# Kernel tuning notes

Hardware: AMD Instinct MI355X
Metric: run time of the kernel (lower is better)

Reference implementation:

```python
import jax, jax.numpy as jnp
import numpy as np

S = 3        # num_scale
C = 256      # codebook / feature dim
K = 512      # codebook size


def _bilinear_down(x, f):
    # torch F.interpolate(scale_factor=1/f, mode='bilinear', align_corners=False)
    # for even integer f: src = (i+0.5)*f - 0.5 = f*i + (f//2 - 1) + 0.5 -> avg of 2 neighbors.
    o = f // 2 - 1
    x = (x[:, :, o::f, :] + x[:, :, o + 1::f, :]) * 0.5
    x = (x[:, :, :, o::f] + x[:, :, :, o + 1::f]) * 0.5
    return x


def _encode(img, w, b):
    # stride-4 patchify conv: (b,3,H,W) -> (b,C,H/4,W/4), NCHW
    y = jax.lax.conv_general_dilated(img, w, (4, 4), 'VALID',
                                     dimension_numbers=('NCHW', 'OIHW', 'NCHW'))
    return y + b[None, :, None, None]


def _match(e, cb):
    # e [..., c], cb [K, c]. logits = -||e - cb||^2; zsoft = softmax(logits).
    # Only max-prob and argmax are consumed downstream, so compute them stably.
    d = (jnp.sum(e * e, -1, keepdims=True)
         - 2.0 * jnp.einsum('...c,kc->...k', e, cb)
         + jnp.sum(cb * cb, -1))
    logits = -d
    zidx = jnp.argmax(logits, -1)
    maxprob = jnp.exp(jnp.max(logits, -1) - jax.scipy.special.logsumexp(logits, -1))
    return maxprob, zidx


def _resample(e, j, i):
    # e is NHWC at scale j; bring it to scale i (avg_pool if j<i, nearest upsample if j>i)
    if j == i:
        return e
    if j < i:
        f = 2 ** (i - j)
        b, h, w, c = e.shape
        return e.reshape(b, h // f, f, w // f, f, c).mean(axis=(2, 4))
    f = 2 ** (j - i)
    return jnp.repeat(jnp.repeat(e, f, axis=1), f, axis=2)


def setup_inputs() -> dict:
    key = jax.random.key(0)
    k1, k2, k3 = jax.random.split(key, 3)
    image = jax.random.normal(k1, (8, 3, 256, 256), jnp.float32)
    conv_w = jax.random.normal(k2, (C, 3, 4, 4), jnp.float32) * 0.05
    conv_b = jnp.zeros((C,), jnp.float32)
    codebooks = jax.random.normal(k3, (1 + S, K, C), jnp.float32) * 0.05
    return {"image": image, "conv_w": conv_w, "conv_b": conv_b, "codebooks": codebooks}


def reference(image, conv_w, conv_b, codebooks):
    # multi-scale inputs (bilinear downsample), shared encoder per scale
    imgs = [image] + [_bilinear_down(image, 2 ** k) for k in range(1, S)]
    encodes = [_encode(im, conv_w, conv_b) for im in imgs]          # NCHW, sizes 64/32/16
    enc_nhwc = [jnp.transpose(e, (0, 2, 3, 1)) for e in encodes]

    cb0 = codebooks[0]
    # ms_fuse, scale i1 = 0 (only scale 0 is returned when decode=None, retr=True):
    stack = jnp.stack([_resample(enc_nhwc[j], j, 0) for j in range(S)])  # [s,b,h,w,c]
    prob1, idx1 = _match(stack, cb0)                                      # [s,b,h,w]
    sel = jnp.argmax(prob1, 0)                                            # [b,h,w] best scale
    zidx1 = jnp.take_along_axis(idx1, sel[None], 0)[0]                    # [b,h,w]
    enc1 = jnp.take_along_axis(stack, sel[None, ..., None], 0)[0]         # [b,h,w,c]
    quant1 = cb0[zidx1]

    # per-scale quantizer for scale 0
    _, zidx2 = _match(enc_nhwc[0], codebooks[1])
    quant2 = codebooks[1][zidx2]

    zidx0 = jnp.stack([zidx1, zidx2], -1)            # [b,h,w,2]
    e_fused = (enc1 + enc_nhwc[0]) * 0.5
    q_fused = (quant1 + quant2) * 0.5
    # alpha = 0 -> residual == quant; naive STE
    ste0 = e_fused + jax.lax.stop_gradient(q_fused - e_fused)

    return (encodes[0],
            jnp.transpose(zidx0, (0, 3, 1, 2)),
            jnp.transpose(ste0, (0, 3, 1, 2)))
```

## Files before the change

### kernel.cpp

```cpp
#include <hip/hip_runtime.h>
#include <math.h>


#define FEAT_OFF   0
#define PART_OFF   11010048
#define PROB_OFF   13434880
#define IDX1_OFF   13477888
#define IDX2_OFF   13520896
#define CNF_OFF    13553664
#define CND_OFF    13554688
#define CBS_OFF    13556736
#define IMG1_OFF   13818880
#define IMG2_OFF   14212096
#define RLIST_OFF  14310400
#define DLIST_OFF  14386176
#define CNT_OFF    14418944

#define PLANE_STRIDE 11010048

#define EPS_V 1e-3f
#define EPS_P_REL 2e-3f

typedef __attribute__((ext_vector_type(8))) short short8;
typedef __attribute__((ext_vector_type(4))) float f32x4;

__device__ inline unsigned short f2bf(float x) {
    unsigned u = __float_as_uint(x);
    return (unsigned short)((u + 0x7FFFu + ((u >> 16) & 1u)) >> 16);
}
__device__ inline float bf2f(unsigned short h) {
    return __uint_as_float(((unsigned)h) << 16);
}
__device__ inline int rswz(int row) { return (row & 3) ^ ((row >> 2) & 3); }

__device__ inline void glds16(const unsigned short* g, unsigned short* l) {
    __builtin_amdgcn_global_load_lds(
        (const __attribute__((address_space(1))) void*)g,
        (__attribute__((address_space(3))) void*)l, 16, 0, 0);
}

__global__ void zero_cnt(int* cnt) { if (threadIdx.x < 2) cnt[threadIdx.x] = 0; }

__global__ void ds_kernel(const float* __restrict__ img, float* __restrict__ out,
                          int Hout, int Wout, int o, int f) {
    int i = blockIdx.x * blockDim.x + threadIdx.x;
    if (i >= 8 * 3 * Hout * Wout) return;
    int x = i % Wout;
    int t = i / Wout;
    int y = t % Hout;
    int bc = t / Hout;
    const float* base = img + ((size_t)bc * 256 + (size_t)(y * f + o)) * 256;
    int cx = x * f + o;
    float v00 = base[cx],     v10 = base[256 + cx];
    float v01 = base[cx + 1], v11 = base[256 + cx + 1];
    out[i] = ((v00 + v10) * 0.5f + (v01 + v11) * 0.5f) * 0.5f;
}

__global__ void cnorm_kernel(const float* __restrict__ cb, double* __restrict__ cnd,
                             float* __restrict__ cnf) {
    int row = blockIdx.x;
    const float* p = cb + (size_t)row * 256;
    int lane = threadIdx.x;
    double s = 0.0;
    for (int c = lane; c < 256; c += 64) {
        double v = (double)p[c];
        s = fma(v, v, s);
    }
    #pragma unroll
    for (int off = 32; off; off >>= 1) s += __shfl_down(s, off);
    if (lane == 0) { cnd[row] = s; cnf[row] = (float)s; }
}

__global__ void split_cb(const float* __restrict__ codebooks, unsigned short* __restrict__ cbs) {
    int i = blockIdx.x * 256 + threadIdx.x;
    if (i >= 262144) return;
    int book = i >> 17, rem = i & 131071;
    int code = rem >> 8, ch = rem & 255;
    float c = codebooks[(size_t)book * 131072 + rem];
    unsigned short h0 = f2bf(c);
    unsigned short h1 = f2bf(c - bf2f(h0));
    int codeblk = code >> 7, row = code & 127;
    int kc = ch >> 5, q = (ch >> 3) & 3, j = ch & 7;
    int qs = q ^ rswz(row);
    size_t off = ((((size_t)(book * 2) * 4 + codeblk) * 8 + kc) * 128 + row) * 32 + qs * 8 + j;
    cbs[off] = h0;
    cbs[off + 4 * 32768] = h1;
}

__launch_bounds__(256)
__global__ void encode_all(const float* __restrict__ image,
                           const float* __restrict__ img1,
                           const float* __restrict__ img2,
                           const float* __restrict__ w,
                           const float* __restrict__ bias,
                           float* __restrict__ feat,
                           unsigned short* __restrict__ featbf) {
    __shared__ float patch[12 * 256];
    __shared__ __align__(16) unsigned short pk[2][2][256];
    int bid = blockIdx.x;
    const float* img; int Hout, rowbase, local;
    if (bid < 512)      { img = image; Hout = 64; rowbase = 0;     local = bid; }
    else if (bid < 768) { img = img1;  Hout = 32; rowbase = 32768; local = bid - 512; }
    else                { img = img2;  Hout = 16; rowbase = 40960; local = bid - 768; }
    int Wout = Hout;
    int tid = threadIdx.x;
    int b = local / Hout, y = local % Hout;
    int Himg = Hout * 4, Wimg = Wout * 4;

    const float* ibase = img + (size_t)b * 3 * Himg * Wimg;
    int nload = 12 * Wimg;
    for (int i = tid; i < nload; i += 256) {
        int col = i % Wimg, r = i / Wimg;
        int ci = r >> 2, kh = r & 3;
        patch[r * Wimg + col] = ibase[((size_t)ci * Himg + 4 * y + kh) * Wimg + col];
    }
    float wr[48];
    #pragma unroll
    for (int j = 0; j < 48; j++) wr[j] = w[tid * 48 + j];
    float bv = bias[tid];
    __syncthreads();

    int wp = tid >> 5, wkc = (tid >> 2) & 7, wg = tid & 3;
    int rb = rowbase + (b * Hout + y) * Wout;
    for (int x = 0; x < Wout; x++) {
        float acc = 0.f;
        #pragma unroll
        for (int ci = 0; ci < 3; ci++)
            #pragma unroll
            for (int kh = 0; kh < 4; kh++) {
                const float* pr = &patch[(ci * 4 + kh) * Wimg + 4 * x];
                #pragma unroll
                for (int kw = 0; kw < 4; kw++)
                    acc = fmaf(pr[kw], wr[ci * 16 + kh * 4 + kw], acc);
            }
        float val = acc + bv;
        int r = rb + x;
        feat[(size_t)r * 256 + tid] = val;
        unsigned short hi = f2bf(val);
        unsigned short lo = f2bf(val - bf2f(hi));
        int bufx = x & 1;
        pk[bufx][0][tid] = hi;
        pk[bufx][1][tid] = lo;
        __syncthreads();
        if (tid < 64) {
            int rowblk = r >> 7, rrow = r & 127;
            int ch0 = wkc * 32 + ((wg ^ rswz(rrow)) << 3);
            uint4 v = *(const uint4*)&pk[bufx][wp][ch0];
            size_t off = ((((size_t)rowblk * 8 + wkc) * 128 + rrow) * 32 + wg * 8)
                         + (size_t)wp * PLANE_STRIDE;
            *(uint4*)&featbf[off] = v;
        }
    }
}

__launch_bounds__(256, 2)
__global__ void match_bulk(const unsigned short* __restrict__ featbf,
                           const unsigned short* __restrict__ cbs,
                           const float* __restrict__ cnf,
                           float* __restrict__ partials) {
    __shared__ unsigned short A0s[2][4096], A1s[2][4096], B0s[2][4096], B1s[2][4096];
    int bid0 = blockIdx.x;
    int bid = (bid0 & 7) * 296 + (bid0 >> 3);
    int codeblk = bid & 3, rowtile = bid >> 2;
    int book = (rowtile >= 336) ? 1 : 0;
    int rowblk = book ? rowtile - 336 : rowtile;
    int vr0 = rowtile * 128;
    int tid = threadIdx.x;
    int wid = tid >> 6, l = tid & 63;
    int waveY = wid & 1, waveX = wid >> 1;
    int lm = l & 15, lq = l >> 4;
    int slot = lq ^ rswz(lm);
    int wlds = wid * 512;

    int kbase = codeblk * 128 + waveX * 64 + lq * 4;
    float4 cnv4[4];
    #pragma unroll
    for (int ct = 0; ct < 4; ct++)
        cnv4[ct] = *(const float4*)&cnf[book * 512 + kbase + ct * 16];

    f32x4 acc[4][4];
    #pragma unroll
    for (int ct = 0; ct < 4; ct++)
        #pragma unroll
        for (int rt = 0; rt < 4; rt++) acc[ct][rt] = (f32x4)0.0f;

    const unsigned short* gA0 = featbf + (size_t)rowblk * 32768 + tid * 8;
    const unsigned short* gA1 = gA0 + PLANE_STRIDE;
    const unsigned short* gB0 = cbs + ((size_t)(book * 8) + codeblk) * 32768 + tid * 8;
    const unsigned short* gB1 = gB0 + 4 * 32768;

    auto STAGE = [&](int buf, int kc) {
        const unsigned short* ga0 = gA0 + kc * 4096;
        const unsigned short* ga1 = gA1 + kc * 4096;
        const unsigned short* gb0 = gB0 + kc * 4096;
        const unsigned short* gb1 = gB1 + kc * 4096;
        #pragma unroll
        for (int i = 0; i < 2; i++) {
            glds16(ga0 + i * 2048, &A0s[buf][i * 2048 + wlds]);
            glds16(ga1 + i * 2048, &A1s[buf][i * 2048 + wlds]);
            glds16(gb0 + i * 2048, &B0s[buf][i * 2048 + wlds]);
            glds16(gb1 + i * 2048, &B1s[buf][i * 2048 + wlds]);
        }
    };

    short8 a0[4], a1[4], b0[4], b1[4];
    auto LOADFRAG = [&](int cur) {
        #pragma unroll
        for (int t = 0; t < 4; t++) {
            int ra = (waveY * 64 + t * 16 + lm) * 32 + slot * 8;
            int rbx = (waveX * 64 + t * 16 + lm) * 32 + slot * 8;
            a0[t] = *(const short8*)&A0s[cur][ra];
            a1[t] = *(const short8*)&A1s[cur][ra];
            b0[t] = *(const short8*)&B0s[cur][rbx];
            b1[t] = *(const short8*)&B1s[cur][rbx];
        }
    };
    auto DOMFMA = [&]() {
        __builtin_amdgcn_s_setprio(1);
        #pragma unroll
        for (int ct = 0; ct < 4; ct++)
            #pragma unroll
            for (int rt = 0; rt < 4; rt++) {
                acc[ct][rt] = __builtin_amdgcn_mfma_f32_16x16x32_bf16(b0[ct], a0[rt], acc[ct][rt], 0, 0, 0);
                acc[ct][rt] = __builtin_amdgcn_mfma_f32_16x16x32_bf16(b1[ct], a0[rt], acc[ct][rt], 0, 0, 0);
                acc[ct][rt] = __builtin_amdgcn_mfma_f32_16x16x32_bf16(b0[ct], a1[rt], acc[ct][rt], 0, 0, 0);
            }
        __builtin_amdgcn_s_setprio(0);
    };

    STAGE(0, 0);
    STAGE(1, 1);

#define MB_STEP(KC)                                                        \
    do {                                                                   \
        asm volatile("s_waitcnt vmcnt(8)" ::: "memory");                   \
        __builtin_amdgcn_s_barrier();                                      \
        __builtin_amdgcn_sched_barrier(0);                                 \
        LOADFRAG((KC) & 1);                                                \
        asm volatile("s_waitcnt lgkmcnt(0)" ::: "memory");                 \
        __builtin_amdgcn_sched_barrier(0);                                 \
        __builtin_amdgcn_s_barrier();                                      \
        __builtin_amdgcn_sched_barrier(0);                                 \
        STAGE((KC) & 1, (KC) + 2);                                         \
        DOMFMA();                                                          \
    } while (0)

    MB_STEP(0); MB_STEP(1); MB_STEP(2); MB_STEP(3); MB_STEP(4); MB_STEP(5);

    asm volatile("s_waitcnt vmcnt(8)" ::: "memory");
    __builtin_amdgcn_s_barrier();
    __builtin_amdgcn_sched_barrier(0);
    LOADFRAG(0);
    DOMFMA();
    asm volatile("s_waitcnt vmcnt(0)" ::: "memory");
    __builtin_amdgcn_s_barrier();
    __builtin_amdgcn_sched_barrier(0);
    LOADFRAG(1);
    DOMFMA();
#undef MB_STEP

    float4* part4 = (float4*)partials;
    #pragma unroll
    for (int rt = 0; rt < 4; rt++) {
        float v[4][4];
        #pragma unroll
        for (int ct = 0; ct < 4; ct++) {
            v[ct][0] = 2.0f * acc[ct][rt][0] - cnv4[ct].x;
            v[ct][1] = 2.0f * acc[ct][rt][1] - cnv4[ct].y;
            v[ct][2] = 2.0f * acc[ct][rt][2] - cnv4[ct].z;
            v[ct][3] = 2.0f * acc[ct][rt][3] - cnv4[ct].w;
        }
        float m1 = v[0][0], m2 = -3.4e38f;
        int k1 = kbase;
        #pragma unroll
        for (int ct = 0; ct < 4; ct++)
            #pragma unroll
            for (int j = 0; j < 4; j++) {
                if (ct == 0 && j == 0) continue;
                float val = v[ct][j];
                if (val > m1) { m2 = m1; m1 = val; k1 = kbase + ct * 16 + j; }
                else m2 = fmaxf(m2, val);
            }
        #pragma unroll
        for (int off = 16; off < 64; off <<= 1) {
            float mo1 = __shfl_xor(m1, off);
            float mo2 = __shfl_xor(m2, off);
            int ko1 = __shfl_xor(k1, off);
            if (mo1 > m1 || (mo1 == m1 && ko1 < k1)) { m2 = fmaxf(m1, mo2); m1 = mo1; k1 = ko1; }
            else m2 = fmaxf(m2, mo1);
        }
        float s = 0.f;
        if (!book) {
            #pragma unroll
            for (int ct = 0; ct < 4; ct++)
                #pragma unroll
                for (int j = 0; j < 4; j++) s += __expf(v[ct][j] - m1);
            #pragma unroll
            for (int off = 16; off < 64; off <<= 1) s += __shfl_xor(s, off);
        }
        if (lq == 0) {
            int vr = vr0 + waveY * 64 + rt * 16 + lm;
            float4 st = make_float4(m1, m2, __int_as_float(k1), s);
            part4[(size_t)vr * 8 + codeblk * 2 + waveX] = st;
        }
    }
}

__global__ void combine_rows(const float* __restrict__ partials,
                             int* __restrict__ idx1, int* __restrict__ idx2,
                             float* __restrict__ prob,
                             int* __restrict__ rlist, int* __restrict__ cnt) {
    int vr = blockIdx.x * 256 + threadIdx.x;
    const float4* p = (const float4*)partials + (size_t)vr * 8;
    float sm[8], ss[8];
    float4 a = p[0];
    float m1 = a.x, m2 = a.y; int k1 = __float_as_int(a.z);
    sm[0] = a.x; ss[0] = a.w;
    #pragma unroll
    for (int j = 1; j < 8; j++) {
        float4 b = p[j];
        sm[j] = b.x; ss[j] = b.w;
        int kk = __float_as_int(b.z);
        if (b.x > m1 || (b.x == m1 && kk < k1)) { m2 = fmaxf(m1, b.y); m1 = b.x; k1 = kk; }
        else m2 = fmaxf(m2, b.x);
    }
    float S = 0.f;
    #pragma unroll
    for (int j = 0; j < 8; j++) S += ss[j] * __expf(sm[j] - m1);
    if (vr < 43008) { idx1[vr] = k1; prob[vr] = 1.0f / S; }
    else idx2[vr - 43008] = k1;
    if (m1 - m2 < EPS_V) { int pos = atomicAdd(cnt, 1); rlist[pos] = vr; }
}

__launch_bounds__(256)
__global__ void rescue_exact(const float* __restrict__ feat,
                             const float* __restrict__ codebooks,
                             const double* __restrict__ cnd,
                             const int* __restrict__ rlist, const int* __restrict__ cnt,
                             int* __restrict__ idx1, int* __restrict__ idx2,
                             float* __restrict__ prob) {
    __shared__ double sfd[256];
    __shared__ double rv[4]; __shared__ int rk[4]; __shared__ double rs[4];
    __shared__ double gvmax; __shared__ int gkmax;
    int tid = threadIdx.x;
    int lane = tid & 63, wave = tid >> 6;
    int n = cnt[0];
    for (int e = blockIdx.x; e < n; e += gridDim.x) {
        int vr = rlist[e];
        int book = vr >= 43008;
        int fr = book ? vr - 43008 : vr;
        sfd[tid] = (double)feat[(size_t)fr * 256 + tid];
        __syncthreads();
        const float* cb = codebooks + (size_t)book * 131072;
        double vloc[2]; int kk[2];
        #pragma unroll
        for (int h = 0; h < 2; h++) {
            int k = h * 256 + tid;
            const float* cp = cb + (size_t)k * 256;
            double dot = 0.0;
            for (int c = 0; c < 256; c++) dot = fma((double)cp[c], sfd[c], dot);
            vloc[h] = 2.0 * dot - cnd[book * 512 + k];
            kk[h] = k;
        }
        double bv = vloc[0]; int bk = kk[0];
        if (vloc[1] > bv || (vloc[1] == bv && kk[1] < bk)) { bv = vloc[1]; bk = kk[1]; }
        #pragma unroll
        for (int off = 32; off; off >>= 1) {
            double vo = __shfl_xor(bv, off);
            int ko = __shfl_xor(bk, off);
            if (vo > bv || (vo == bv && ko < bk)) { bv = vo; bk = ko; }
        }
        if (lane == 0) { rv[wave] = bv; rk[wave] = bk; }
        __syncthreads();
        if (tid == 0) {
            double v0 = rv[0]; int K = rk[0];
            #pragma unroll
            for (int w = 1; w < 4; w++)
                if (rv[w] > v0 || (rv[w] == v0 && rk[w] < K)) { v0 = rv[w]; K = rk[w]; }
            gvmax = v0; gkmax = K;
        }
        __syncthreads();
        double vm = gvmax;
        double s = exp(vloc[0] - vm) + exp(vloc[1] - vm);
        #pragma unroll
        for (int off = 32; off; off >>= 1) s += __shfl_xor(s, off);
        if (lane == 0) rs[wave] = s;
        __syncthreads();
        if (tid == 0) {
            double S = ((rs[0] + rs[1]) + rs[2]) + rs[3];
            if (book) idx2[fr] = gkmax;
            else { idx1[vr] = gkmax; prob[vr] = (float)(1.0 / S); }
        }
        __syncthreads();
    }
}

__launch_bounds__(256)
__global__ void fuse1(const float* __restrict__ feat,
                      const float* __restrict__ prob,
                      const int* __restrict__ idx1, const int* __restrict__ idx2,
                      const float* __restrict__ codebooks,
                      float* __restrict__ out0, float* __restrict__ outZ,
                      float* __restrict__ outS,
                      int* __restrict__ dlist, int* __restrict__ cnt) {
    __shared__ int rsel_s[64], i1_s[64], i2_s[64], defer_s[64];
    int tid = threadIdx.x;
    int b = blockIdx.x >> 6, y = blockIdx.x & 63;

    if (tid < 64) {
        int x = tid;
        int r0 = (b * 64 + y) * 64 + x;
        int r1 = 32768 + (b * 32 + (y >> 1)) * 32 + (x >> 1);
        int r2 = 40960 + (b * 16 + (y >> 2)) * 16 + (x >> 2);
        float p0 = prob[r0], p1 = prob[r1], p2 = prob[r2];
        int rsel = r0; float best = p0;
        if (p1 > best) { best = p1; rsel = r1; }
        if (p2 > best) { best = p2; rsel = r2; }
        float second = (rsel == r0) ? fmaxf(p1, p2)
                     : (rsel == r1) ? fmaxf(p0, p2) : fmaxf(p0, p1);
        int defer = (best - second < EPS_P_REL * best) ? 1 : 0;
        defer_s[x] = defer;
        if (defer) {
            int pos = atomicAdd(cnt + 1, 1);
            dlist[pos] = (b << 12) | (y << 6) | x;
            rsel_s[x] = r0; i1_s[x] = 0; i2_s[x] = 0;
        } else {
            int i1 = idx1[rsel], i2 = idx2[r0];
            rsel_s[x] = rsel; i1_s[x] = i1; i2_s[x] = i2;
            size_t zb = (size_t)b * 8192 + (size_t)y * 64 + x;
            outZ[zb] = (float)i1;
            outZ[zb + 4096] = (float)i2;
        }
    }
    __syncthreads();

    int x = tid & 63, cc = tid >> 6;
    int r0 = (b * 64 + y) * 64 + x;
    const float* e0p = feat + (size_t)r0 * 256;
    const float* e1p = feat + (size_t)rsel_s[x] * 256;
    const float* q1p = codebooks + (size_t)i1_s[x] * 256;
    const float* q2p = codebooks + (size_t)(512 + i2_s[x]) * 256;
    int defer = defer_s[x];
    for (int it = 0; it < 16; it++) {
        int c = it * 16 + cc * 4;
        float4 e0 = *(const float4*)&e0p[c];
        size_t o = (((size_t)b * 256 + c) * 64 + y) * 64 + x;
        out0[o]         = e0.x;
        out0[o + 4096]  = e0.y;
        out0[o + 8192]  = e0.z;
        out0[o + 12288] = e0.w;
        if (!defer) {
            float4 e1 = *(const float4*)&e1p[c];
            float4 q1 = *(const float4*)&q1p[c];
            float4 q2 = *(const float4*)&q2p[c];
            float ef, qf;
            ef = (e1.x + e0.x) * 0.5f; qf = (q1.x + q2.x) * 0.5f; outS[o]         = ef + (qf - ef);
            ef = (e1.y + e0.y) * 0.5f; qf = (q1.y + q2.y) * 0.5f; outS[o + 4096]  = ef + (qf - ef);
            ef = (e1.z + e0.z) * 0.5f; qf = (q1.z + q2.z) * 0.5f; outS[o + 8192]  = ef + (qf - ef);
            ef = (e1.w + e0.w) * 0.5f; qf = (q1.w + q2.w) * 0.5f; outS[o + 12288] = ef + (qf - ef);
        }
    }
}

__launch_bounds__(256)
__global__ void fuse2(const float* __restrict__ feat,
                      const float* __restrict__ codebooks,
                      const double* __restrict__ cnd,
                      const int* __restrict__ idx2,
                      const int* __restrict__ dlist, const int* __restrict__ cnt,
                      float* __restrict__ outZ, float* __restrict__ outS) {
    __shared__ double sfd[256];
    __shared__ double rv[4]; __shared__ int rk[4]; __shared__ double rs[4];
    __shared__ double gvmax;
    __shared__ double pRes[3]; __shared__ int kRes[3];
    __shared__ int selS, i2S;
    int tid = threadIdx.x;
    int lane = tid & 63, wave = tid >> 6;
    int n = cnt[1];
    for (int e = blockIdx.x; e < n; e += gridDim.x) {
        int px = dlist[e];
        int b = px >> 12, y = (px >> 6) & 63, x = px & 63;
        int r0 = (b * 64 + y) * 64 + x;
        int r1 = 32768 + (b * 32 + (y >> 1)) * 32 + (x >> 1);
        int r2 = 40960 + (b * 16 + (y >> 2)) * 16 + (x >> 2);
        int rows[3] = {r0, r1, r2};
        for (int s3 = 0; s3 < 3; s3++) {
            sfd[tid] = (double)feat[(size_t)rows[s3] * 256 + tid];
            __syncthreads();
            double vloc[2];
            #pragma unroll
            for (int h = 0; h < 2; h++) {
                int k = h * 256 + tid;
                const float* cp = codebooks + (size_t)k * 256;
                double dot = 0.0;
                for (int c = 0; c < 256; c++) dot = fma((double)cp[c], sfd[c], dot);
                vloc[h] = 2.0 * dot - cnd[k];
            }
            double bv = vloc[0]; int bk = tid;
            if (vloc[1] > bv) { bv = vloc[1]; bk = tid + 256; }
            #pragma unroll
            for (int off = 32; off; off >>= 1) {
                double vo = __shfl_xor(bv, off);
                int ko = __shfl_xor(bk, off);
                if (vo > bv || (vo == bv && ko < bk)) { bv = vo; bk = ko; }
            }
            if (lane == 0) { rv[wave] = bv; rk[wave] = bk; }
            __syncthreads();
            if (tid == 0) {
                double v0 = rv[0]; int K = rk[0];
                #pragma unroll
                for (int w = 1; w < 4; w++)
                    if (rv[w] > v0 || (rv[w] == v0 && rk[w] < K)) { v0 = rv[w]; K = rk[w]; }
                gvmax = v0; kRes[s3] = K;
            }
            __syncthreads();
            double vm = gvmax;
            double s = exp(vloc[0] - vm) + exp(vloc[1] - vm);
            #pragma unroll
            for (int off = 32; off; off >>= 1) s += __shfl_xor(s, off);
            if (lane == 0) rs[wave] = s;
            __syncthreads();
            if (tid == 0) pRes[s3] = 1.0 / (((rs[0] + rs[1]) + rs[2]) + rs[3]);
            __syncthreads();
        }
        if (tid == 0) {
            int sel = 0; double best = pRes[0];
            if (pRes[1] > best) { best = pRes[1]; sel = 1; }
            if (pRes[2] > best) { best = pRes[2]; sel = 2; }
            selS = sel;
            int i2 = idx2[r0];
            i2S = i2;
            size_t zb = (size_t)b * 8192 + (size_t)y * 64 + x;
            outZ[zb] = (float)kRes[sel];
            outZ[zb + 4096] = (float)i2;
        }
        __syncthreads();
        int sel = selS;
        int c = tid;
        float e0 = feat[(size_t)r0 * 256 + c];
        float e1 = feat[(size_t)rows[sel] * 256 + c];
        float q1 = codebooks[(size_t)kRes[sel] * 256 + c];
        float q2 = codebooks[(size_t)(512 + i2S) * 256 + c];
        float ef = (e1 + e0) * 0.5f;
        float qf = (q1 + q2) * 0.5f;
        size_t o = (((size_t)b * 256 + c) * 64 + y) * 64 + x;
        outS[o] = ef + (qf - ef);
        __syncthreads();
    }
}

extern "C" void kernel_launch(void* const* d_in, const int* in_sizes, int n_in,
                              void* d_out, int out_size, void* d_ws, size_t ws_size,
                              hipStream_t stream) {
    (void)in_sizes; (void)n_in; (void)out_size; (void)ws_size;
    const float* image     = (const float*)d_in[0];
    const float* conv_w    = (const float*)d_in[1];
    const float* conv_b    = (const float*)d_in[2];
    const float* codebooks = (const float*)d_in[3];

    float*  ws    = (float*)d_ws;
    float*  feat  = ws + FEAT_OFF;
    float*  parts = ws + PART_OFF;
    float*  prob  = ws + PROB_OFF;
    int*    idx1  = (int*)(ws + IDX1_OFF);
    int*    idx2  = (int*)(ws + IDX2_OFF);
    float*  cnf   = ws + CNF_OFF;
    double* cnd   = (double*)(ws + CND_OFF);
    unsigned short* cbs = (unsigned short*)(ws + CBS_OFF);
    float*  img1  = ws + IMG1_OFF;
    float*  img2  = ws + IMG2_OFF;
    int*    rlist = (int*)(ws + RLIST_OFF);
    int*    dlist = (int*)(ws + DLIST_OFF);
    int*    cnt   = (int*)(ws + CNT_OFF);

    float* out  = (float*)d_out;
    float* out0 = out;
    float* outZ = out + 8388608;
    float* outS = out + 8454144;
    unsigned short* featbf = (unsigned short*)d_out;

    zero_cnt<<<1, 64, 0, stream>>>(cnt);
    ds_kernel<<<1536, 256, 0, stream>>>(image, img1, 128, 128, 0, 2);
    ds_kernel<<<384, 256, 0, stream>>>(image, img2, 64, 64, 1, 4);
    cnorm_kernel<<<1024, 64, 0, stream>>>(codebooks, cnd, cnf);
    split_cb<<<1024, 256, 0, stream>>>(codebooks, cbs);
    encode_all<<<896, 256, 0, stream>>>(image, img1, img2, conv_w, conv_b, feat, featbf);
    match_bulk<<<2368, 256, 0, stream>>>(featbf, cbs, cnf, parts);
    combine_rows<<<296, 256, 0, stream>>>(parts, idx1, idx2, prob, rlist, cnt);
    rescue_exact<<<1024, 256, 0, stream>>>(feat, codebooks, cnd, rlist, cnt, idx1, idx2, prob);
    fuse1<<<512, 256, 0, stream>>>(feat, prob, idx1, idx2, codebooks, out0, outZ, outS, dlist, cnt);
    fuse2<<<512, 256, 0, stream>>>(feat, codebooks, cnd, idx2, dlist, cnt, outZ, outS);
}
```

Measured before the change: 299.8 us.

## Fuse prep kernels, batch encode stores, stream B1 via registers, vectorize rescue dots

Merges the zero/downsample/cnorm/split launches into one prep kernel to cut launch overhead. The encoder now computes four pixels per barrier instead of one. match_bulk drops the B1 shared-memory buffer and loads that plane straight into registers with inline asm, raising occupancy to three blocks per SM. The fp64 rescue loops use float4 loads with four accumulators. The inline-asm waitcnt accounting is delicate, and splitting the dot into four accumulators can change fp64 rounding slightly.

```diff
diff --git a/kernel.cpp b/kernel.cpp
--- a/kernel.cpp
+++ b/kernel.cpp
@@ -23,6 +23,7 @@
 
 typedef __attribute__((ext_vector_type(8))) short short8;
 typedef __attribute__((ext_vector_type(4))) float f32x4;
+typedef __attribute__((ext_vector_type(4))) unsigned int u32x4;
 
 __device__ inline unsigned short f2bf(float x) {
     unsigned u = __float_as_uint(x);
@@ -39,52 +40,62 @@
         (__attribute__((address_space(3))) void*)l, 16, 0, 0);
 }
 
-__global__ void zero_cnt(int* cnt) { if (threadIdx.x < 2) cnt[threadIdx.x] = 0; }
-
-__global__ void ds_kernel(const float* __restrict__ img, float* __restrict__ out,
-                          int Hout, int Wout, int o, int f) {
-    int i = blockIdx.x * blockDim.x + threadIdx.x;
-    if (i >= 8 * 3 * Hout * Wout) return;
-    int x = i % Wout;
-    int t = i / Wout;
-    int y = t % Hout;
-    int bc = t / Hout;
-    const float* base = img + ((size_t)bc * 256 + (size_t)(y * f + o)) * 256;
-    int cx = x * f + o;
-    float v00 = base[cx],     v10 = base[256 + cx];
-    float v01 = base[cx + 1], v11 = base[256 + cx + 1];
-    out[i] = ((v00 + v10) * 0.5f + (v01 + v11) * 0.5f) * 0.5f;
-}
-
-__global__ void cnorm_kernel(const float* __restrict__ cb, double* __restrict__ cnd,
-                             float* __restrict__ cnf) {
-    int row = blockIdx.x;
-    const float* p = cb + (size_t)row * 256;
-    int lane = threadIdx.x;
-    double s = 0.0;
-    for (int c = lane; c < 256; c += 64) {
-        double v = (double)p[c];
-        s = fma(v, v, s);
-    }
-    #pragma unroll
-    for (int off = 32; off; off >>= 1) s += __shfl_down(s, off);
-    if (lane == 0) { cnd[row] = s; cnf[row] = (float)s; }
-}
-
-__global__ void split_cb(const float* __restrict__ codebooks, unsigned short* __restrict__ cbs) {
-    int i = blockIdx.x * 256 + threadIdx.x;
-    if (i >= 262144) return;
-    int book = i >> 17, rem = i & 131071;
-    int code = rem >> 8, ch = rem & 255;
-    float c = codebooks[(size_t)book * 131072 + rem];
-    unsigned short h0 = f2bf(c);
-    unsigned short h1 = f2bf(c - bf2f(h0));
-    int codeblk = code >> 7, row = code & 127;
-    int kc = ch >> 5, q = (ch >> 3) & 3, j = ch & 7;
-    int qs = q ^ rswz(row);
-    size_t off = ((((size_t)(book * 2) * 4 + codeblk) * 8 + kc) * 128 + row) * 32 + qs * 8 + j;
-    cbs[off] = h0;
-    cbs[off + 4 * 32768] = h1;
+__launch_bounds__(256)
+__global__ void prep(const float* __restrict__ image,
+                     const float* __restrict__ codebooks,
+                     float* __restrict__ img1, float* __restrict__ img2,
+                     double* __restrict__ cnd, float* __restrict__ cnf,
+                     unsigned short* __restrict__ cbs, int* __restrict__ cnt) {
+    int bid = blockIdx.x, tid = threadIdx.x;
+    if (bid == 0 && tid < 2) cnt[tid] = 0;
+    if (bid < 1536) {
+        int i = bid * 256 + tid;
+        int x = i & 127;
+        int t = i >> 7;
+        int y = t & 127;
+        int bc = t >> 7;
+        const float* base = image + ((size_t)bc * 256 + (size_t)(y * 2)) * 256;
+        int cx = x * 2;
+        float v00 = base[cx],     v10 = base[256 + cx];
+        float v01 = base[cx + 1], v11 = base[256 + cx + 1];
+        img1[i] = ((v00 + v10) * 0.5f + (v01 + v11) * 0.5f) * 0.5f;
+    } else if (bid < 1920) {
+        int i = (bid - 1536) * 256 + tid;
+        int x = i & 63;
+        int t = i >> 6;
+        int y = t & 63;
+        int bc = t >> 6;
+        const float* base = image + ((size_t)bc * 256 + (size_t)(y * 4 + 1)) * 256;
+        int cx = x * 4 + 1;
+        float v00 = base[cx],     v10 = base[256 + cx];
+        float v01 = base[cx + 1], v11 = base[256 + cx + 1];
+        img2[i] = ((v00 + v10) * 0.5f + (v01 + v11) * 0.5f) * 0.5f;
+    } else if (bid < 2176) {
+        int row = (bid - 1920) * 4 + (tid >> 6);
+        int lane = tid & 63;
+        const float* p = codebooks + (size_t)row * 256;
+        double s = 0.0;
+        for (int c = lane; c < 256; c += 64) {
+            double v = (double)p[c];
+            s = fma(v, v, s);
+        }
+        #pragma unroll
+        for (int off = 32; off; off >>= 1) s += __shfl_down(s, off);
+        if (lane == 0) { cnd[row] = s; cnf[row] = (float)s; }
+    } else {
+        int i = (bid - 2176) * 256 + tid;
+        int book = i >> 17, rem = i & 131071;
+        int code = rem >> 8, ch = rem & 255;
+        float c = codebooks[(size_t)book * 131072 + rem];
+        unsigned short h0 = f2bf(c);
+        unsigned short h1 = f2bf(c - bf2f(h0));
+        int codeblk = code >> 7, row = code & 127;
+        int kc = ch >> 5, q = (ch >> 3) & 3, j = ch & 7;
+        int qs = q ^ rswz(row);
+        size_t off = ((((size_t)(book * 2) * 4 + codeblk) * 8 + kc) * 128 + row) * 32 + qs * 8 + j;
+        cbs[off] = h0;
+        cbs[off + 4 * 32768] = h1;
+    }
 }
 
 __launch_bounds__(256)
@@ -96,7 +107,7 @@
                            float* __restrict__ feat,
                            unsigned short* __restrict__ featbf) {
     __shared__ float patch[12 * 256];
-    __shared__ __align__(16) unsigned short pk[2][2][256];
+    __shared__ __align__(16) unsigned short pk[2][4][2][256];
     int bid = blockIdx.x;
     const float* img; int Hout, rowbase, local;
     if (bid < 512)      { img = image; Hout = 64; rowbase = 0;     local = bid; }
@@ -120,45 +131,48 @@
     float bv = bias[tid];
     __syncthreads();
 
-    int wp = tid >> 5, wkc = (tid >> 2) & 7, wg = tid & 3;
+    int fp = tid >> 6, fwp = (tid >> 5) & 1, fkc = (tid >> 2) & 7, fwg = tid & 3;
     int rb = rowbase + (b * Hout + y) * Wout;
-    for (int x = 0; x < Wout; x++) {
-        float acc = 0.f;
-        #pragma unroll
-        for (int ci = 0; ci < 3; ci++)
-            #pragma unroll
-            for (int kh = 0; kh < 4; kh++) {
-                const float* pr = &patch[(ci * 4 + kh) * Wimg + 4 * x];
+    for (int x0 = 0; x0 < Wout; x0 += 4) {
+        int buf = (x0 >> 2) & 1;
+        #pragma unroll
+        for (int p = 0; p < 4; p++) {
+            int x = x0 + p;
+            float acc = 0.f;
+            #pragma unroll
+            for (int ci = 0; ci < 3; ci++)
                 #pragma unroll
-                for (int kw = 0; kw < 4; kw++)
-                    acc = fmaf(pr[kw], wr[ci * 16 + kh * 4 + kw], acc);
-            }
-        float val = acc + bv;
-        int r = rb + x;
-        feat[(size_t)r * 256 + tid] = val;
-        unsigned short hi = f2bf(val);
-        unsigned short lo = f2bf(val - bf2f(hi));
-        int bufx = x & 1;
-        pk[bufx][0][tid] = hi;
-        pk[bufx][1][tid] = lo;
-        __syncthreads();
-        if (tid < 64) {
+                for (int kh = 0; kh < 4; kh++) {
+                    const float* pr = &patch[(ci * 4 + kh) * Wimg + 4 * x];
+                    #pragma unroll
+                    for (int kw = 0; kw < 4; kw++)
+                        acc = fmaf(pr[kw], wr[ci * 16 + kh * 4 + kw], acc);
+                }
+            float val = acc + bv;
+            feat[(size_t)(rb + x) * 256 + tid] = val;
+            unsigned short hi = f2bf(val);
+            pk[buf][p][0][tid] = hi;
+            pk[buf][p][1][tid] = f2bf(val - bf2f(hi));
+        }
+        __syncthreads();
+        {
+            int r = rb + x0 + fp;
             int rowblk = r >> 7, rrow = r & 127;
-            int ch0 = wkc * 32 + ((wg ^ rswz(rrow)) << 3);
-            uint4 v = *(const uint4*)&pk[bufx][wp][ch0];
-            size_t off = ((((size_t)rowblk * 8 + wkc) * 128 + rrow) * 32 + wg * 8)
-                         + (size_t)wp * PLANE_STRIDE;
+            int ch0 = fkc * 32 + ((fwg ^ rswz(rrow)) << 3);
+            uint4 v = *(const uint4*)&pk[buf][fp][fwp][ch0];
+            size_t off = (((size_t)rowblk * 8 + fkc) * 128 + rrow) * 32 + fwg * 8
+                       + (size_t)fwp * PLANE_STRIDE;
             *(uint4*)&featbf[off] = v;
         }
     }
 }
 
-__launch_bounds__(256, 2)
+__launch_bounds__(256, 3)
 __global__ void match_bulk(const unsigned short* __restrict__ featbf,
                            const unsigned short* __restrict__ cbs,
                            const float* __restrict__ cnf,
                            float* __restrict__ partials) {
-    __shared__ unsigned short A0s[2][4096], A1s[2][4096], B0s[2][4096], B1s[2][4096];
+    __shared__ unsigned short A0s[2][4096], A1s[2][4096], B0s[2][4096];
     int bid0 = blockIdx.x;
     int bid = (bid0 & 7) * 296 + (bid0 >> 3);
     int codeblk = bid & 3, rowtile = bid >> 2;
@@ -172,12 +186,6 @@
     int slot = lq ^ rswz(lm);
     int wlds = wid * 512;
 
-    int kbase = codeblk * 128 + waveX * 64 + lq * 4;
-    float4 cnv4[4];
-    #pragma unroll
-    for (int ct = 0; ct < 4; ct++)
-        cnv4[ct] = *(const float4*)&cnf[book * 512 + kbase + ct * 16];
-
     f32x4 acc[4][4];
     #pragma unroll
     for (int ct = 0; ct < 4; ct++)
@@ -187,23 +195,35 @@
     const unsigned short* gA0 = featbf + (size_t)rowblk * 32768 + tid * 8;
     const unsigned short* gA1 = gA0 + PLANE_STRIDE;
     const unsigned short* gB0 = cbs + ((size_t)(book * 8) + codeblk) * 32768 + tid * 8;
-    const unsigned short* gB1 = gB0 + 4 * 32768;
-
-    auto STAGE = [&](int buf, int kc) {
+    const unsigned short* gB1f = cbs + ((size_t)(book * 8) + codeblk) * 32768 + 131072
+                               + ((waveX * 64 + lm) * 32 + slot * 8);
+
+    auto STAGE6 = [&](int buf, int kc) {
         const unsigned short* ga0 = gA0 + kc * 4096;
         const unsigned short* ga1 = gA1 + kc * 4096;
         const unsigned short* gb0 = gB0 + kc * 4096;
-        const unsigned short* gb1 = gB1 + kc * 4096;
         #pragma unroll
         for (int i = 0; i < 2; i++) {
             glds16(ga0 + i * 2048, &A0s[buf][i * 2048 + wlds]);
             glds16(ga1 + i * 2048, &A1s[buf][i * 2048 + wlds]);
             glds16(gb0 + i * 2048, &B0s[buf][i * 2048 + wlds]);
-            glds16(gb1 + i * 2048, &B1s[buf][i * 2048 + wlds]);
         }
     };
 
-    short8 a0[4], a1[4], b0[4], b1[4];
+    u32x4 qA[4], qB[4];
+    auto B1LOAD = [&](u32x4 (&q)[4], int kc) {
+        const unsigned short* p = gB1f + (size_t)kc * 4096;
+        asm volatile(
+            "global_load_dwordx4 %0, %4, off\n\t"
+            "global_load_dwordx4 %1, %4, off offset:1024\n\t"
+            "global_load_dwordx4 %2, %4, off offset:2048\n\t"
+            "global_load_dwordx4 %3, %4, off offset:3072"
+            : "=&v"(q[0]), "=&v"(q[1]), "=&v"(q[2]), "=&v"(q[3])
+            : "v"(p)
+            : "memory");
+    };
+
+    short8 a0[4], a1[4], b0[4];
     auto LOADFRAG = [&](int cur) {
         #pragma unroll
         for (int t = 0; t < 4; t++) {
@@ -212,28 +232,30 @@
             a0[t] = *(const short8*)&A0s[cur][ra];
             a1[t] = *(const short8*)&A1s[cur][ra];
             b0[t] = *(const short8*)&B0s[cur][rbx];
-            b1[t] = *(const short8*)&B1s[cur][rbx];
         }
     };
-    auto DOMFMA = [&]() {
+    auto DOMFMA = [&](u32x4 (&q)[4]) {
         __builtin_amdgcn_s_setprio(1);
         #pragma unroll
-        for (int ct = 0; ct < 4; ct++)
+        for (int ct = 0; ct < 4; ct++) {
+            short8 b1v;
+            __builtin_memcpy(&b1v, &q[ct], 16);
             #pragma unroll
             for (int rt = 0; rt < 4; rt++) {
                 acc[ct][rt] = __builtin_amdgcn_mfma_f32_16x16x32_bf16(b0[ct], a0[rt], acc[ct][rt], 0, 0, 0);
-                acc[ct][rt] = __builtin_amdgcn_mfma_f32_16x16x32_bf16(b1[ct], a0[rt], acc[ct][rt], 0, 0, 0);
+                acc[ct][rt] = __builtin_amdgcn_mfma_f32_16x16x32_bf16(b1v,    a0[rt], acc[ct][rt], 0, 0, 0);
                 acc[ct][rt] = __builtin_amdgcn_mfma_f32_16x16x32_bf16(b0[ct], a1[rt], acc[ct][rt], 0, 0, 0);
             }
+        }
         __builtin_amdgcn_s_setprio(0);
     };
 
-    STAGE(0, 0);
-    STAGE(1, 1);
-
-#define MB_STEP(KC)                                                        \
+    STAGE6(0, 0); B1LOAD(qA, 0);
+    STAGE6(1, 1); B1LOAD(qB, 1);
+
+#define MB_STEP(KC, QQ)                                                    \
     do {                                                                   \
-        asm volatile("s_waitcnt vmcnt(8)" ::: "memory");                   \
+        asm volatile("s_waitcnt vmcnt(10)" ::: "memory");                  \
         __builtin_amdgcn_s_barrier();                                      \
         __builtin_amdgcn_sched_barrier(0);                                 \
         LOADFRAG((KC) & 1);                                                \
@@ -241,25 +263,37 @@
         __builtin_amdgcn_sched_barrier(0);                                 \
         __builtin_amdgcn_s_barrier();                                      \
         __builtin_amdgcn_sched_barrier(0);                                 \
-        STAGE((KC) & 1, (KC) + 2);                                         \
-        DOMFMA();                                                          \
+        STAGE6((KC) & 1, (KC) + 2);                                        \
+        DOMFMA(QQ);                                                        \
+        B1LOAD(QQ, (KC) + 2);                                              \
     } while (0)
 
-    MB_STEP(0); MB_STEP(1); MB_STEP(2); MB_STEP(3); MB_STEP(4); MB_STEP(5);
-
-    asm volatile("s_waitcnt vmcnt(8)" ::: "memory");
+    MB_STEP(0, qA); MB_STEP(1, qB); MB_STEP(2, qA);
+    MB_STEP(3, qB); MB_STEP(4, qA); MB_STEP(5, qB);
+#undef MB_STEP
+
+    asm volatile("s_waitcnt vmcnt(10)" ::: "memory");
     __builtin_amdgcn_s_barrier();
     __builtin_amdgcn_sched_barrier(0);
     LOADFRAG(0);
-    DOMFMA();
+    asm volatile("s_waitcnt lgkmcnt(0)" ::: "memory");
+    __builtin_amdgcn_sched_barrier(0);
+    DOMFMA(qA);
     asm volatile("s_waitcnt vmcnt(0)" ::: "memory");
     __builtin_amdgcn_s_barrier();
     __builtin_amdgcn_sched_barrier(0);
     LOADFRAG(1);
-    DOMFMA();
-#undef MB_STEP
-
+    asm volatile("s_waitcnt lgkmcnt(0)" ::: "memory");
+    __builtin_amdgcn_sched_barrier(0);
+    DOMFMA(qB);
+
+    int kbase = codeblk * 128 + waveX * 64 + lq * 4;
+    float4 cnv4[4];
+    #pragma unroll
+    for (int ct = 0; ct < 4; ct++)
+        cnv4[ct] = *(const float4*)&cnf[book * 512 + kbase + ct * 16];
     float4* part4 = (float4*)partials;
+
     #pragma unroll
     for (int rt = 0; rt < 4; rt++) {
         float v[4][4];
@@ -357,8 +391,15 @@
         for (int h = 0; h < 2; h++) {
             int k = h * 256 + tid;
             const float* cp = cb + (size_t)k * 256;
-            double dot = 0.0;
-            for (int c = 0; c < 256; c++) dot = fma((double)cp[c], sfd[c], dot);
+            double d0 = 0.0, d1 = 0.0, d2 = 0.0, d3 = 0.0;
+            for (int c = 0; c < 256; c += 4) {
+                float4 cv = *(const float4*)&cp[c];
+                d0 = fma((double)cv.x, sfd[c],     d0);
+                d1 = fma((double)cv.y, sfd[c + 1], d1);
+                d2 = fma((double)cv.z, sfd[c + 2], d2);
+                d3 = fma((double)cv.w, sfd[c + 3], d3);
+            }
+            double dot = (d0 + d1) + (d2 + d3);
             vloc[h] = 2.0 * dot - cnd[book * 512 + k];
             kk[h] = k;
         }
@@ -492,8 +533,15 @@
             for (int h = 0; h < 2; h++) {
                 int k = h * 256 + tid;
                 const float* cp = codebooks + (size_t)k * 256;
-                double dot = 0.0;
-                for (int c = 0; c < 256; c++) dot = fma((double)cp[c], sfd[c], dot);
+                double d0 = 0.0, d1 = 0.0, d2 = 0.0, d3 = 0.0;
+                for (int c = 0; c < 256; c += 4) {
+                    float4 cv = *(const float4*)&cp[c];
+                    d0 = fma((double)cv.x, sfd[c],     d0);
+                    d1 = fma((double)cv.y, sfd[c + 1], d1);
+                    d2 = fma((double)cv.z, sfd[c + 2], d2);
+                    d3 = fma((double)cv.w, sfd[c + 3], d3);
+                }
+                double dot = (d0 + d1) + (d2 + d3);
                 vloc[h] = 2.0 * dot - cnd[k];
             }
             double bv = vloc[0]; int bk = tid;
@@ -579,11 +627,7 @@
     float* outS = out + 8454144;
     unsigned short* featbf = (unsigned short*)d_out;
 
-    zero_cnt<<<1, 64, 0, stream>>>(cnt);
-    ds_kernel<<<1536, 256, 0, stream>>>(image, img1, 128, 128, 0, 2);
-    ds_kernel<<<384, 256, 0, stream>>>(image, img2, 64, 64, 1, 4);
-    cnorm_kernel<<<1024, 64, 0, stream>>>(codebooks, cnd, cnf);
-    split_cb<<<1024, 256, 0, stream>>>(codebooks, cbs);
+    prep<<<3200, 256, 0, stream>>>(image, codebooks, img1, img2, cnd, cnf, cbs, cnt);
     encode_all<<<896, 256, 0, stream>>>(image, img1, img2, conv_w, conv_b, feat, featbf);
     match_bulk<<<2368, 256, 0, stream>>>(featbf, cbs, cnf, parts);
     combine_rows<<<296, 256, 0, stream>>>(parts, idx1, idx2, prob, rlist, cnt);
```

Result: faster. 283.8 us (-5.3%).
